# Performance work log

Hardware: AMD Instinct MI355X
Metric: run time of the kernel (lower is better)

The kernel has to match this reference:

```python
import jax, jax.numpy as jnp
import numpy as np

B, S, D, H, E, N = 4, 1024, 1024, 4096, 1024, 8


def setup_inputs() -> dict:
    key = jax.random.key(0)
    ks = jax.random.split(key, 5)
    x = jax.random.normal(ks[0], (B, S, D), jnp.float32)
    # Learned parameters (Linear weights stored as [in, out] for x @ W)
    Wg = jax.random.normal(ks[1], (D, N), jnp.float32) * 0.02
    bg = jnp.zeros((N,), jnp.float32)
    W1 = jax.random.normal(ks[2], (N, D, H), jnp.float32) * 0.02
    b1 = jnp.zeros((N, H), jnp.float32)
    W2 = jax.random.normal(ks[3], (N, H, E), jnp.float32) * 0.02
    b2 = jnp.zeros((N, E), jnp.float32)
    return {"x": x, "Wg": Wg, "bg": bg, "W1": W1, "b1": b1,
            "W2": W2, "b2": b2, "num_experts_per_tok": 2}


def reference(x, Wg, bg, W1, b1, W2, b2, num_experts_per_tok):
    # Gating: softmax over experts
    gate_probs = jax.nn.softmax(x @ Wg + bg, axis=-1)            # [B,S,N]
    n_exp = gate_probs.shape[-1]
    # Top-k routing mask (indices are distinct, so summed one-hots == scatter of 1.0)
    _, topk_idx = jax.lax.top_k(gate_probs, num_experts_per_tok)  # [B,S,k]
    mask = jax.nn.one_hot(topk_idx, n_exp, dtype=gate_probs.dtype).sum(axis=-2)  # [B,S,N]
    gated = gate_probs * mask
    # F.normalize(p=1): divide by max(L1-norm, eps)
    gated = gated / jnp.maximum(jnp.sum(jnp.abs(gated), axis=-1, keepdims=True), 1e-12)
    # Dense all-expert FFN (matches torch.stack over ModuleList)
    h = jax.nn.relu(jnp.einsum('bsd,ndh->bsnh', x, W1) + b1)      # [B,S,N,H]
    expert_out = jnp.einsum('bsnh,nhe->bsne', h, W2) + b2          # [B,S,N,E]
    out = jnp.einsum('bsn,bsne->bse', gated, expert_out)           # [B,S,E]
    # Auxiliary load-balancing stats
    tokens = float(x.shape[0] * x.shape[1])
    importance = gate_probs.sum(axis=(0, 1)) / tokens              # [N]
    load = mask.sum(axis=(0, 1)) / tokens                          # [N]
    lb_loss = (n_exp * (importance * load).sum()).astype(out.dtype)
    return out, lb_loss, importance, load
```

## Files before the change

### kernel.cpp

```cpp
#include <hip/hip_runtime.h>

#define TOKENS 4096
#define DDIM 1024
#define HDIM 4096
#define EDIM 1024
#define NEXP 8
#define SLOTS (TOKENS * 2)
#define OUT_MAIN ((size_t)TOKENS * EDIM)

typedef __bf16 bf16_t;
typedef bf16_t bf16x8 __attribute__((ext_vector_type(8)));
typedef float f32x4 __attribute__((ext_vector_type(4)));

__device__ __forceinline__ unsigned short f32_to_bf16(float f) {
  union { float f; unsigned u; } v; v.f = f;
  unsigned r = v.u + 0x7FFFu + ((v.u >> 16) & 1u);
  return (unsigned short)(r >> 16);
}

__device__ __forceinline__ void gload_lds16(const void* g, void* l) {
  __builtin_amdgcn_global_load_lds(
      (__attribute__((address_space(1))) void*)(g),
      (__attribute__((address_space(3))) void*)(l), 16, 0, 0);
}

__global__ __launch_bounds__(256) void gate_kernel(
    const float* __restrict__ x, const float* __restrict__ Wg,
    const float* __restrict__ bg, unsigned short* __restrict__ xb,
    int2* __restrict__ tok_e, float2* __restrict__ tok_w,
    float* __restrict__ probs) {
  const int wave = threadIdx.x >> 6;
  const int lane = threadIdx.x & 63;
  const int t = blockIdx.x * 4 + wave;
  const float4* xr = reinterpret_cast<const float4*>(x + (size_t)t * DDIM);
  ushort4* xbr = reinterpret_cast<ushort4*>(xb + (size_t)t * DDIM);

  float acc[NEXP];
#pragma unroll
  for (int n = 0; n < NEXP; n++) acc[n] = 0.f;

#pragma unroll
  for (int i = 0; i < 4; i++) {
    int d4 = lane + 64 * i;
    float4 xv = xr[d4];
    ushort4 o;
    o.x = f32_to_bf16(xv.x); o.y = f32_to_bf16(xv.y);
    o.z = f32_to_bf16(xv.z); o.w = f32_to_bf16(xv.w);
    xbr[d4] = o;
    const float* wrow = Wg + (size_t)d4 * 4 * NEXP;
#pragma unroll
    for (int n = 0; n < NEXP; n++)
      acc[n] += xv.x * wrow[n] + xv.y * wrow[NEXP + n] +
                xv.z * wrow[2 * NEXP + n] + xv.w * wrow[3 * NEXP + n];
  }
#pragma unroll
  for (int n = 0; n < NEXP; n++)
#pragma unroll
    for (int m = 32; m > 0; m >>= 1) acc[n] += __shfl_xor(acc[n], m, 64);

  if (lane == 0) {
    float p[NEXP];
    float mx = -1e30f;
#pragma unroll
    for (int n = 0; n < NEXP; n++) { p[n] = acc[n] + bg[n]; mx = fmaxf(mx, p[n]); }
    float s = 0.f;
#pragma unroll
    for (int n = 0; n < NEXP; n++) { p[n] = expf(p[n] - mx); s += p[n]; }
    float inv = 1.f / s;
#pragma unroll
    for (int n = 0; n < NEXP; n++) { p[n] *= inv; probs[(size_t)t * NEXP + n] = p[n]; }
    int e1 = 0; float p1 = p[0];
#pragma unroll
    for (int n = 1; n < NEXP; n++) if (p[n] > p1) { p1 = p[n]; e1 = n; }
    int e2 = (e1 == 0) ? 1 : 0; float p2 = p[e2];
#pragma unroll
    for (int n = 0; n < NEXP; n++) if (n != e1 && p[n] > p2) { p2 = p[n]; e2 = n; }
    float denom = p1 + p2;
    tok_e[t] = make_int2(e1, e2);
    tok_w[t] = make_float2(p1 / denom, p2 / denom);
  }
}

__global__ __launch_bounds__(1024) void route_kernel(
    const int2* __restrict__ tok_e, const float2* __restrict__ tok_w,
    int* __restrict__ offs_g, int* __restrict__ counts_g,
    int* __restrict__ token_ids, float* __restrict__ slot_w) {
  __shared__ int cnt[NEXP];
  __shared__ int offs[NEXP + 1];
  __shared__ int cur[NEXP];
  const int tid = threadIdx.x;
  if (tid < NEXP) cnt[tid] = 0;
  __syncthreads();
  int2 e[4]; float2 w[4];
#pragma unroll
  for (int i = 0; i < 4; i++) {
    int t = tid + 1024 * i;
    e[i] = tok_e[t]; w[i] = tok_w[t];
    atomicAdd(&cnt[e[i].x], 1);
    atomicAdd(&cnt[e[i].y], 1);
  }
  __syncthreads();
  if (tid == 0) {
    int s = 0;
#pragma unroll
    for (int n = 0; n < NEXP; n++) { offs[n] = s; cur[n] = s; s += cnt[n]; }
    offs[NEXP] = s;
  }
  __syncthreads();
  if (tid < NEXP) { offs_g[tid] = offs[tid]; counts_g[tid] = cnt[tid]; }
  if (tid == 0) offs_g[NEXP] = offs[NEXP];
#pragma unroll
  for (int i = 0; i < 4; i++) {
    int t = tid + 1024 * i;
    int s0 = atomicAdd(&cur[e[i].x], 1);
    token_ids[s0] = t; slot_w[s0] = w[i].x;
    int s1 = atomicAdd(&cur[e[i].y], 1);
    token_ids[s1] = t; slot_w[s1] = w[i].y;
  }
}

__global__ __launch_bounds__(256) void transpose_convert_kernel(
    const float* __restrict__ src, unsigned short* __restrict__ dst, int R, int C) {
  __shared__ float tile[32][33];
  const size_t mat = (size_t)R * C;
  const float* s = src + (size_t)blockIdx.z * mat;
  unsigned short* d = dst + (size_t)blockIdx.z * mat;
  int c0 = blockIdx.x * 32, r0 = blockIdx.y * 32;
  int tx = threadIdx.x, ty = threadIdx.y;
#pragma unroll
  for (int i = 0; i < 32; i += 8)
    tile[ty + i][tx] = s[(size_t)(r0 + ty + i) * C + (c0 + tx)];
  __syncthreads();
#pragma unroll
  for (int i = 0; i < 32; i += 8)
    d[(size_t)(c0 + ty + i) * R + (r0 + tx)] = f32_to_bf16(tile[tx][ty + i]);
}

__global__ __launch_bounds__(256) void gemm1_kernel(
    const unsigned short* __restrict__ xb, const unsigned short* __restrict__ w1t,
    const float* __restrict__ b1, const int* __restrict__ token_ids,
    const int* __restrict__ offs, unsigned short* __restrict__ h) {
  const int e = blockIdx.z;
  const int off0 = offs[e];
  const int ne = offs[e + 1] - off0;
  const int mt = blockIdx.y;
  if (mt * 128 >= ne) return;
  const int nt = blockIdx.x;

  __shared__ unsigned short As[128 * 32];
  __shared__ unsigned short Bs[128 * 32];

  const int tid = threadIdx.x;
  const int lane = tid & 63;
  const int wave = tid >> 6;
  const int wm = (wave >> 1) * 64;
  const int wn = (wave & 1) * 64;

  const int srow = tid >> 2;
  const int sk = (tid & 3) * 8;
  int lrow0 = mt * 128 + srow;
  int lrow1 = lrow0 + 64;
  int slot0 = off0 + min(lrow0, ne - 1);
  int slot1 = off0 + min(lrow1, ne - 1);
  const unsigned short* gA0 = xb + (size_t)token_ids[slot0] * DDIM + sk;
  const unsigned short* gA1 = xb + (size_t)token_ids[slot1] * DDIM + sk;
  const unsigned short* wbase = w1t + (size_t)e * HDIM * DDIM;
  const unsigned short* gB0 = wbase + (size_t)(nt * 128 + srow) * DDIM + sk;
  const unsigned short* gB1 = gB0 + (size_t)64 * DDIM;

  unsigned short* lA = As + wave * 512;
  unsigned short* lB = Bs + wave * 512;

  f32x4 acc[4][4];
#pragma unroll
  for (int i = 0; i < 4; i++)
#pragma unroll
    for (int j = 0; j < 4; j++) acc[i][j] = (f32x4)(0.f);

  const int frow = lane & 15;
  const int fk = (lane >> 4) * 8;

  for (int k0 = 0; k0 < DDIM; k0 += 32) {
    __syncthreads();
    gload_lds16(gA0 + k0, lA);
    gload_lds16(gA1 + k0, lA + 2048);
    gload_lds16(gB0 + k0, lB);
    gload_lds16(gB1 + k0, lB + 2048);
    __syncthreads();
    bf16x8 af[4], bfv[4];
#pragma unroll
    for (int mi = 0; mi < 4; mi++)
      af[mi] = *reinterpret_cast<const bf16x8*>(&As[(wm + mi * 16 + frow) * 32 + fk]);
#pragma unroll
    for (int ni = 0; ni < 4; ni++)
      bfv[ni] = *reinterpret_cast<const bf16x8*>(&Bs[(wn + ni * 16 + frow) * 32 + fk]);
#pragma unroll
    for (int mi = 0; mi < 4; mi++)
#pragma unroll
      for (int ni = 0; ni < 4; ni++)
        acc[mi][ni] = __builtin_amdgcn_mfma_f32_16x16x32_bf16(af[mi], bfv[ni], acc[mi][ni], 0, 0, 0);
  }

  const float* b1e = b1 + (size_t)e * HDIM + nt * 128;
  const int r4 = (lane >> 4) * 4;
  const int cb = lane & 15;
#pragma unroll
  for (int mi = 0; mi < 4; mi++) {
#pragma unroll
    for (int r = 0; r < 4; r++) {
      int grow = mt * 128 + wm + mi * 16 + r4 + r;
      if (grow < ne) {
        unsigned short* hr = h + (size_t)(off0 + grow) * HDIM + nt * 128;
#pragma unroll
        for (int ni = 0; ni < 4; ni++) {
          int col = wn + ni * 16 + cb;
          float v = acc[mi][ni][r] + b1e[col];
          hr[col] = f32_to_bf16(fmaxf(v, 0.f));
        }
      }
    }
  }
}

__global__ __launch_bounds__(256) void gemm2_kernel(
    const unsigned short* __restrict__ h, const unsigned short* __restrict__ w2t,
    const float* __restrict__ b2, const int* __restrict__ token_ids,
    const float* __restrict__ slot_w, const int* __restrict__ offs,
    float* __restrict__ out) {
  const int e = blockIdx.z;
  const int off0 = offs[e];
  const int ne = offs[e + 1] - off0;
  const int mt = blockIdx.y;
  if (mt * 128 >= ne) return;
  const int nt = blockIdx.x;

  __shared__ unsigned short As[128 * 32];
  __shared__ unsigned short Bs[128 * 32];

  const int tid = threadIdx.x;
  const int lane = tid & 63;
  const int wave = tid >> 6;
  const int wm = (wave >> 1) * 64;
  const int wn = (wave & 1) * 64;

  const int srow = tid >> 2;
  const int sk = (tid & 3) * 8;
  int lrow0 = mt * 128 + srow;
  int lrow1 = lrow0 + 64;
  int slot0 = off0 + min(lrow0, ne - 1);
  int slot1 = off0 + min(lrow1, ne - 1);
  const unsigned short* gA0 = h + (size_t)slot0 * HDIM + sk;
  const unsigned short* gA1 = h + (size_t)slot1 * HDIM + sk;
  const unsigned short* wbase = w2t + (size_t)e * EDIM * HDIM;
  const unsigned short* gB0 = wbase + (size_t)(nt * 128 + srow) * HDIM + sk;
  const unsigned short* gB1 = gB0 + (size_t)64 * HDIM;

  unsigned short* lA = As + wave * 512;
  unsigned short* lB = Bs + wave * 512;

  f32x4 acc[4][4];
#pragma unroll
  for (int i = 0; i < 4; i++)
#pragma unroll
    for (int j = 0; j < 4; j++) acc[i][j] = (f32x4)(0.f);

  const int frow = lane & 15;
  const int fk = (lane >> 4) * 8;

  for (int k0 = 0; k0 < HDIM; k0 += 32) {
    __syncthreads();
    gload_lds16(gA0 + k0, lA);
    gload_lds16(gA1 + k0, lA + 2048);
    gload_lds16(gB0 + k0, lB);
    gload_lds16(gB1 + k0, lB + 2048);
    __syncthreads();
    bf16x8 af[4], bfv[4];
#pragma unroll
    for (int mi = 0; mi < 4; mi++)
      af[mi] = *reinterpret_cast<const bf16x8*>(&As[(wm + mi * 16 + frow) * 32 + fk]);
#pragma unroll
    for (int ni = 0; ni < 4; ni++)
      bfv[ni] = *reinterpret_cast<const bf16x8*>(&Bs[(wn + ni * 16 + frow) * 32 + fk]);
#pragma unroll
    for (int mi = 0; mi < 4; mi++)
#pragma unroll
      for (int ni = 0; ni < 4; ni++)
        acc[mi][ni] = __builtin_amdgcn_mfma_f32_16x16x32_bf16(af[mi], bfv[ni], acc[mi][ni], 0, 0, 0);
  }

  const float* b2e = b2 + (size_t)e * EDIM + nt * 128;
  const int r4 = (lane >> 4) * 4;
  const int cb = lane & 15;
#pragma unroll
  for (int mi = 0; mi < 4; mi++) {
#pragma unroll
    for (int r = 0; r < 4; r++) {
      int grow = mt * 128 + wm + mi * 16 + r4 + r;
      if (grow < ne) {
        int slot = off0 + grow;
        int tokid = token_ids[slot];
        float wgt = slot_w[slot];
        float* orow = out + (size_t)tokid * EDIM + nt * 128;
#pragma unroll
        for (int ni = 0; ni < 4; ni++) {
          int col = wn + ni * 16 + cb;
          float v = (acc[mi][ni][r] + b2e[col]) * wgt;
          atomicAdd(&orow[col], v);
        }
      }
    }
  }
}

__global__ __launch_bounds__(512) void stats_kernel(
    const float* __restrict__ probs, const int* __restrict__ counts,
    float* __restrict__ tail) {
  const int wave = threadIdx.x >> 6;
  const int lane = threadIdx.x & 63;
  float s = 0.f;
  for (int t = lane; t < TOKENS; t += 64) s += probs[(size_t)t * NEXP + wave];
#pragma unroll
  for (int m = 32; m > 0; m >>= 1) s += __shfl_xor(s, m, 64);
  __shared__ float imp_s[NEXP];
  if (lane == 0) imp_s[wave] = s / (float)TOKENS;
  __syncthreads();
  if (threadIdx.x == 0) {
    float lb = 0.f;
#pragma unroll
    for (int n = 0; n < NEXP; n++) {
      float imp = imp_s[n];
      float ld = (float)counts[n] / (float)TOKENS;
      tail[1 + n] = imp;
      tail[1 + NEXP + n] = ld;
      lb += imp * ld;
    }
    tail[0] = (float)NEXP * lb;
  }
}

extern "C" void kernel_launch(void* const* d_in, const int* in_sizes, int n_in,
                              void* d_out, int out_size, void* d_ws, size_t ws_size,
                              hipStream_t stream) {
  const float* x  = (const float*)d_in[0];
  const float* Wg = (const float*)d_in[1];
  const float* bg = (const float*)d_in[2];
  const float* W1 = (const float*)d_in[3];
  const float* b1 = (const float*)d_in[4];
  const float* W2 = (const float*)d_in[5];
  const float* b2 = (const float*)d_in[6];
  float* out = (float*)d_out;
  char* ws = (char*)d_ws;

  const size_t XB_OFF   = 0;
  const size_t W1T_OFF  = XB_OFF + (size_t)TOKENS * DDIM * 2;
  const size_t W2T_OFF  = W1T_OFF + (size_t)NEXP * DDIM * HDIM * 2;
  const size_t H_OFF    = W2T_OFF + (size_t)NEXP * HDIM * EDIM * 2;
  const size_t TOKE_OFF = H_OFF + (size_t)SLOTS * HDIM * 2;
  const size_t TOKW_OFF = TOKE_OFF + (size_t)TOKENS * sizeof(int2);
  const size_t TID_OFF  = TOKW_OFF + (size_t)TOKENS * sizeof(float2);
  const size_t SLW_OFF  = TID_OFF + (size_t)SLOTS * 4;
  const size_t PROB_OFF = SLW_OFF + (size_t)SLOTS * 4;
  const size_t META_OFF = PROB_OFF + (size_t)TOKENS * NEXP * 4;
  const size_t WS_NEED  = META_OFF + 64 * 4;
  if (ws_size < WS_NEED) return;

  unsigned short* xb   = (unsigned short*)(ws + XB_OFF);
  unsigned short* w1t  = (unsigned short*)(ws + W1T_OFF);
  unsigned short* w2t  = (unsigned short*)(ws + W2T_OFF);
  unsigned short* hbuf = (unsigned short*)(ws + H_OFF);
  int2*   tok_e = (int2*)(ws + TOKE_OFF);
  float2* tok_w = (float2*)(ws + TOKW_OFF);
  int*    tids  = (int*)(ws + TID_OFF);
  float*  slw   = (float*)(ws + SLW_OFF);
  float*  probs = (float*)(ws + PROB_OFF);
  int*    counts = (int*)(ws + META_OFF);
  int*    offs   = counts + 8;

  hipMemsetAsync(out, 0, (size_t)out_size * sizeof(float), stream);

  gate_kernel<<<TOKENS / 4, 256, 0, stream>>>(x, Wg, bg, xb, tok_e, tok_w, probs);
  route_kernel<<<1, 1024, 0, stream>>>(tok_e, tok_w, offs, counts, tids, slw);
  transpose_convert_kernel<<<dim3(HDIM / 32, DDIM / 32, NEXP), dim3(32, 8), 0, stream>>>(W1, w1t, DDIM, HDIM);
  transpose_convert_kernel<<<dim3(EDIM / 32, HDIM / 32, NEXP), dim3(32, 8), 0, stream>>>(W2, w2t, HDIM, EDIM);
  gemm1_kernel<<<dim3(HDIM / 128, SLOTS / 128, NEXP), 256, 0, stream>>>(xb, w1t, b1, tids, offs, hbuf);
  gemm2_kernel<<<dim3(EDIM / 128, SLOTS / 128, NEXP), 256, 0, stream>>>(hbuf, w2t, b2, tids, slw, offs, out);
  stats_kernel<<<1, 512, 0, stream>>>(probs, counts, out + OUT_MAIN);
}
```

Baseline: 416.3 us.

## Deepen K tile to 64 with XOR-swizzled LDS and widen gemm2 block tile

```diff
diff --git a/kernel.cpp b/kernel.cpp
--- a/kernel.cpp
+++ b/kernel.cpp
@@ -147,8 +147,8 @@
   if (mt * 128 >= ne) return;
   const int nt = blockIdx.x;
 
-  __shared__ unsigned short As[128 * 32];
-  __shared__ unsigned short Bs[128 * 32];
+  __shared__ unsigned short As[128 * 64];
+  __shared__ unsigned short Bs[128 * 64];
 
   const int tid = threadIdx.x;
   const int lane = tid & 63;
@@ -156,20 +156,18 @@
   const int wm = (wave >> 1) * 64;
   const int wn = (wave & 1) * 64;
 
-  const int srow = tid >> 2;
-  const int sk = (tid & 3) * 8;
-  int lrow0 = mt * 128 + srow;
-  int lrow1 = lrow0 + 64;
-  int slot0 = off0 + min(lrow0, ne - 1);
-  int slot1 = off0 + min(lrow1, ne - 1);
-  const unsigned short* gA0 = xb + (size_t)token_ids[slot0] * DDIM + sk;
-  const unsigned short* gA1 = xb + (size_t)token_ids[slot1] * DDIM + sk;
+  const int prow = tid >> 3;
+  const int krow = (tid & 7) ^ (prow & 7);
+  const unsigned short* gA[4];
+  const unsigned short* gB[4];
   const unsigned short* wbase = w1t + (size_t)e * HDIM * DDIM;
-  const unsigned short* gB0 = wbase + (size_t)(nt * 128 + srow) * DDIM + sk;
-  const unsigned short* gB1 = gB0 + (size_t)64 * DDIM;
-
-  unsigned short* lA = As + wave * 512;
-  unsigned short* lB = Bs + wave * 512;
+#pragma unroll
+  for (int j = 0; j < 4; j++) {
+    int row = prow + j * 32;
+    int slot = off0 + min(mt * 128 + row, ne - 1);
+    gA[j] = xb + (size_t)token_ids[slot] * DDIM + krow * 8;
+    gB[j] = wbase + (size_t)(nt * 128 + row) * DDIM + krow * 8;
+  }
 
   f32x4 acc[4][4];
 #pragma unroll
@@ -178,27 +176,37 @@
     for (int j = 0; j < 4; j++) acc[i][j] = (f32x4)(0.f);
 
   const int frow = lane & 15;
-  const int fk = (lane >> 4) * 8;
-
-  for (int k0 = 0; k0 < DDIM; k0 += 32) {
+  const int q = lane >> 4;
+
+  for (int k0 = 0; k0 < DDIM; k0 += 64) {
     __syncthreads();
-    gload_lds16(gA0 + k0, lA);
-    gload_lds16(gA1 + k0, lA + 2048);
-    gload_lds16(gB0 + k0, lB);
-    gload_lds16(gB1 + k0, lB + 2048);
+#pragma unroll
+    for (int j = 0; j < 4; j++) {
+      gload_lds16(gA[j] + k0, As + j * 2048 + wave * 512);
+      gload_lds16(gB[j] + k0, Bs + j * 2048 + wave * 512);
+    }
     __syncthreads();
-    bf16x8 af[4], bfv[4];
-#pragma unroll
-    for (int mi = 0; mi < 4; mi++)
-      af[mi] = *reinterpret_cast<const bf16x8*>(&As[(wm + mi * 16 + frow) * 32 + fk]);
-#pragma unroll
-    for (int ni = 0; ni < 4; ni++)
-      bfv[ni] = *reinterpret_cast<const bf16x8*>(&Bs[(wn + ni * 16 + frow) * 32 + fk]);
-#pragma unroll
-    for (int mi = 0; mi < 4; mi++)
-#pragma unroll
-      for (int ni = 0; ni < 4; ni++)
-        acc[mi][ni] = __builtin_amdgcn_mfma_f32_16x16x32_bf16(af[mi], bfv[ni], acc[mi][ni], 0, 0, 0);
+#pragma unroll
+    for (int kk = 0; kk < 2; kk++) {
+      bf16x8 af[4], bfv[4];
+#pragma unroll
+      for (int mi = 0; mi < 4; mi++) {
+        int row = wm + mi * 16 + frow;
+        int k16 = (kk * 4 + q) ^ (row & 7);
+        af[mi] = *reinterpret_cast<const bf16x8*>(&As[row * 64 + k16 * 8]);
+      }
+#pragma unroll
+      for (int ni = 0; ni < 4; ni++) {
+        int row = wn + ni * 16 + frow;
+        int k16 = (kk * 4 + q) ^ (row & 7);
+        bfv[ni] = *reinterpret_cast<const bf16x8*>(&Bs[row * 64 + k16 * 8]);
+      }
+#pragma unroll
+      for (int mi = 0; mi < 4; mi++)
+#pragma unroll
+        for (int ni = 0; ni < 4; ni++)
+          acc[mi][ni] = __builtin_amdgcn_mfma_f32_16x16x32_bf16(af[mi], bfv[ni], acc[mi][ni], 0, 0, 0);
+    }
   }
 
   const float* b1e = b1 + (size_t)e * HDIM + nt * 128;
@@ -222,7 +230,7 @@
   }
 }
 
-__global__ __launch_bounds__(256) void gemm2_kernel(
+__global__ __launch_bounds__(512) void gemm2_kernel(
     const unsigned short* __restrict__ h, const unsigned short* __restrict__ w2t,
     const float* __restrict__ b2, const int* __restrict__ token_ids,
     const float* __restrict__ slot_w, const int* __restrict__ offs,
@@ -234,29 +242,31 @@
   if (mt * 128 >= ne) return;
   const int nt = blockIdx.x;
 
-  __shared__ unsigned short As[128 * 32];
-  __shared__ unsigned short Bs[128 * 32];
+  __shared__ unsigned short As[128 * 64];
+  __shared__ unsigned short Bs[256 * 64];
 
   const int tid = threadIdx.x;
   const int lane = tid & 63;
   const int wave = tid >> 6;
-  const int wm = (wave >> 1) * 64;
-  const int wn = (wave & 1) * 64;
-
-  const int srow = tid >> 2;
-  const int sk = (tid & 3) * 8;
-  int lrow0 = mt * 128 + srow;
-  int lrow1 = lrow0 + 64;
-  int slot0 = off0 + min(lrow0, ne - 1);
-  int slot1 = off0 + min(lrow1, ne - 1);
-  const unsigned short* gA0 = h + (size_t)slot0 * HDIM + sk;
-  const unsigned short* gA1 = h + (size_t)slot1 * HDIM + sk;
+  const int wm = (wave >> 2) * 64;
+  const int wn = (wave & 3) * 64;
+
+  const int prow = tid >> 3;
+  const int krow = (tid & 7) ^ (prow & 7);
+  const unsigned short* gA[2];
+  const unsigned short* gB[4];
   const unsigned short* wbase = w2t + (size_t)e * EDIM * HDIM;
-  const unsigned short* gB0 = wbase + (size_t)(nt * 128 + srow) * HDIM + sk;
-  const unsigned short* gB1 = gB0 + (size_t)64 * HDIM;
-
-  unsigned short* lA = As + wave * 512;
-  unsigned short* lB = Bs + wave * 512;
+#pragma unroll
+  for (int j = 0; j < 2; j++) {
+    int row = prow + j * 64;
+    int slot = off0 + min(mt * 128 + row, ne - 1);
+    gA[j] = h + (size_t)slot * HDIM + krow * 8;
+  }
+#pragma unroll
+  for (int j = 0; j < 4; j++) {
+    int row = prow + j * 64;
+    gB[j] = wbase + (size_t)(nt * 256 + row) * HDIM + krow * 8;
+  }
 
   f32x4 acc[4][4];
 #pragma unroll
@@ -265,30 +275,41 @@
     for (int j = 0; j < 4; j++) acc[i][j] = (f32x4)(0.f);
 
   const int frow = lane & 15;
-  const int fk = (lane >> 4) * 8;
-
-  for (int k0 = 0; k0 < HDIM; k0 += 32) {
+  const int q = lane >> 4;
+
+  for (int k0 = 0; k0 < HDIM; k0 += 64) {
     __syncthreads();
-    gload_lds16(gA0 + k0, lA);
-    gload_lds16(gA1 + k0, lA + 2048);
-    gload_lds16(gB0 + k0, lB);
-    gload_lds16(gB1 + k0, lB + 2048);
+#pragma unroll
+    for (int j = 0; j < 2; j++)
+      gload_lds16(gA[j] + k0, As + j * 4096 + wave * 512);
+#pragma unroll
+    for (int j = 0; j < 4; j++)
+      gload_lds16(gB[j] + k0, Bs + j * 4096 + wave * 512);
     __syncthreads();
-    bf16x8 af[4], bfv[4];
-#pragma unroll
-    for (int mi = 0; mi < 4; mi++)
-      af[mi] = *reinterpret_cast<const bf16x8*>(&As[(wm + mi * 16 + frow) * 32 + fk]);
-#pragma unroll
-    for (int ni = 0; ni < 4; ni++)
-      bfv[ni] = *reinterpret_cast<const bf16x8*>(&Bs[(wn + ni * 16 + frow) * 32 + fk]);
-#pragma unroll
-    for (int mi = 0; mi < 4; mi++)
-#pragma unroll
-      for (int ni = 0; ni < 4; ni++)
-        acc[mi][ni] = __builtin_amdgcn_mfma_f32_16x16x32_bf16(af[mi], bfv[ni], acc[mi][ni], 0, 0, 0);
-  }
-
-  const float* b2e = b2 + (size_t)e * EDIM + nt * 128;
+#pragma unroll
+    for (int kk = 0; kk < 2; kk++) {
+      bf16x8 af[4], bfv[4];
+#pragma unroll
+      for (int mi = 0; mi < 4; mi++) {
+        int row = wm + mi * 16 + frow;
+        int k16 = (kk * 4 + q) ^ (row & 7);
+        af[mi] = *reinterpret_cast<const bf16x8*>(&As[row * 64 + k16 * 8]);
+      }
+#pragma unroll
+      for (int ni = 0; ni < 4; ni++) {
+        int row = wn + ni * 16 + frow;
+        int k16 = (kk * 4 + q) ^ (row & 7);
+        bfv[ni] = *reinterpret_cast<const bf16x8*>(&Bs[row * 64 + k16 * 8]);
+      }
+#pragma unroll
+      for (int mi = 0; mi < 4; mi++)
+#pragma unroll
+        for (int ni = 0; ni < 4; ni++)
+          acc[mi][ni] = __builtin_amdgcn_mfma_f32_16x16x32_bf16(af[mi], bfv[ni], acc[mi][ni], 0, 0, 0);
+    }
+  }
+
+  const float* b2e = b2 + (size_t)e * EDIM + nt * 256;
   const int r4 = (lane >> 4) * 4;
   const int cb = lane & 15;
 #pragma unroll
@@ -300,7 +321,7 @@
         int slot = off0 + grow;
         int tokid = token_ids[slot];
         float wgt = slot_w[slot];
-        float* orow = out + (size_t)tokid * EDIM + nt * 128;
+        float* orow = out + (size_t)tokid * EDIM + nt * 256;
 #pragma unroll
         for (int ni = 0; ni < 4; ni++) {
           int col = wn + ni * 16 + cb;
@@ -383,6 +404,6 @@
   transpose_convert_kernel<<<dim3(HDIM / 32, DDIM / 32, NEXP), dim3(32, 8), 0, stream>>>(W1, w1t, DDIM, HDIM);
   transpose_convert_kernel<<<dim3(EDIM / 32, HDIM / 32, NEXP), dim3(32, 8), 0, stream>>>(W2, w2t, HDIM, EDIM);
   gemm1_kernel<<<dim3(HDIM / 128, SLOTS / 128, NEXP), 256, 0, stream>>>(xb, w1t, b1, tids, offs, hbuf);
-  gemm2_kernel<<<dim3(EDIM / 128, SLOTS / 128, NEXP), 256, 0, stream>>>(hbuf, w2t, b2, tids, slw, offs, out);
+  gemm2_kernel<<<dim3(EDIM / 256, SLOTS / 128, NEXP), 512, 0, stream>>>(hbuf, w2t, b2, tids, slw, offs, out);
   stats_kernel<<<1, 512, 0, stream>>>(probs, counts, out + OUT_MAIN);
 }
```

Result: slower. 486.5 us (+16.9%).
